# Performance work log

Measured on AMD Instinct MI355X. Metric: run time of the kernel, lower is better.

Reference implementation:

```python
import jax, jax.numpy as jnp
import numpy as np


def setup_inputs() -> dict:
    key = jax.random.key(0)
    k1, k2, k3, k4, k5, k6 = jax.random.split(key, 6)
    B, V = 128, 128000
    logits = jax.random.normal(k1, (B, V), dtype=jnp.float32) * 2.0
    # keep temperatures away from 0 to avoid overflow in logits/temp
    temperatures = 0.7 + 0.6 * jax.random.uniform(k2, (B,), dtype=jnp.float32)
    top_ks = jax.random.randint(k3, (B,), 1, 1024, dtype=jnp.int32)
    top_ps = 0.7 + 0.29 * jax.random.uniform(k4, (B,), dtype=jnp.float32)
    min_ps = 0.02 * jax.random.uniform(k5, (B,), dtype=jnp.float32)
    # uniform variate for inverse-CDF multinomial sampling (one sample per row)
    u = jax.random.uniform(k6, (B, 1), dtype=jnp.float32)
    return {
        "logits": logits,
        "temperatures": temperatures,
        "top_ks": top_ks,
        "top_ps": top_ps,
        "min_ps": min_ps,
        "u": u,
    }


def reference(logits, temperatures, top_ks, top_ps, min_ps, u):
    """Faithful jax version of Sampler's torch-native sampling path:
    softmax(logits/T) -> descending sort -> top-k mask -> top-p mask
    (cumsum computed pre-mask, exactly as torch code) -> min-p mask ->
    multinomial sample (inverse CDF with provided uniform u) ->
    gather original token index. Also returns the renormalized filtered
    probs scattered back to vocab order (top_p_normalize_probs-style)."""
    B, V = logits.shape
    probs = jax.nn.softmax(logits / temperatures[:, None], axis=-1)  # [B, V]

    order = jnp.argsort(-probs, axis=-1)                     # descending indices
    probs_sort = jnp.take_along_axis(probs, order, axis=-1)  # [B, V] sorted desc
    probs_sum = jnp.cumsum(probs_sort, axis=-1)              # cumsum BEFORE masking

    pos = jnp.arange(V, dtype=jnp.int32)[None, :]
    # top-k: zero everything at rank >= top_k
    probs_sort = jnp.where(pos >= top_ks[:, None], 0.0, probs_sort)
    # top-p: zero where cumulative mass strictly before this token exceeds top_p
    probs_sort = jnp.where(probs_sum - probs_sort > top_ps[:, None], 0.0, probs_sort)
    # min-p: threshold relative to the max prob (rank-0 entry survives both masks)
    min_p_thr = probs_sort[:, :1] * min_ps[:, None]
    probs_sort = jnp.where(probs_sort < min_p_thr, 0.0, probs_sort)

    total = jnp.sum(probs_sort, axis=-1, keepdims=True)      # [B, 1]
    cdf = jnp.cumsum(probs_sort, axis=-1) / total            # normalized CDF
    # inverse-CDF sampling == torch.multinomial(probs_sort, 1)
    sampled_rank = jnp.clip(jnp.sum(cdf < u, axis=-1, keepdims=True), 0, V - 1)
    token_ids = jnp.take_along_axis(order, sampled_rank, axis=-1)[:, 0].astype(jnp.int32)

    # scatter renormalized filtered probs back to original vocab positions
    inv_order = jnp.argsort(order, axis=-1)
    norm_probs = jnp.take_along_axis(probs_sort / total, inv_order, axis=-1)
    return token_ids, norm_probs
```

## Files before the change

kernel.cpp:

```cpp
#include <hip/hip_runtime.h>
#include <stdint.h>
#include <math.h>

#define T0 256
#define T1 512
#define TPB 1024
#define NB 2048
#define SPLIT 8
#define LCAND 1024
#define CAND2 2048
#define PS0 2048
#define L2E 1.44269504088896f

typedef float vfloat4 __attribute__((ext_vector_type(4)));
typedef unsigned long long ull;

__device__ __forceinline__ unsigned fkey(float f) {
    unsigned u = __float_as_uint(f);
    return (u & 0x80000000u) ? ~u : (u | 0x80000000u);
}
__device__ __forceinline__ float funkey(unsigned k) {
    unsigned u = (k & 0x80000000u) ? (k ^ 0x80000000u) : ~k;
    return __uint_as_float(u);
}
__device__ __forceinline__ ull packkv(unsigned k, unsigned idx) {
    return ((ull)k << 32) | (ull)(~idx);
}

__device__ __forceinline__ void suffix_scan_2048(unsigned* h, unsigned* wscr, int tid)
{
    const int lane = tid & 63, w = tid >> 6;
    const int i0 = 2047 - 2 * tid;
    const int i1 = 2046 - 2 * tid;
    unsigned a = h[i0], b = h[i1];
    unsigned s = a + b;
    unsigned inc = s;
    #pragma unroll
    for (int d = 1; d < 64; d <<= 1) { unsigned o = __shfl_up(inc, d); if (lane >= d) inc += o; }
    if (lane == 63) wscr[w] = inc;
    __syncthreads();
    if (w == 0) {
        unsigned v = (lane < 16) ? wscr[lane] : 0u;
        unsigned vi = v;
        #pragma unroll
        for (int d = 1; d < 16; d <<= 1) { unsigned o = __shfl_up(vi, d); if (lane >= d) vi += o; }
        if (lane < 16) wscr[16 + lane] = vi - v;
    }
    __syncthreads();
    unsigned off = wscr[16 + w] + (inc - s);
    h[i0] = off + a;
    h[i1] = off + a + b;
    __syncthreads();
}

__global__ __launch_bounds__(T0)
void k0_cut(const float* __restrict__ logits,
            const float* __restrict__ temps,
            const int* __restrict__ top_ks,
            float* __restrict__ ws_cy,
            unsigned* __restrict__ ws_cut,
            int V, int Vq)
{
    const int slot = blockIdx.x;
    const int b = slot / SPLIT, s = slot % SPLIT;
    const int tid = threadIdx.x, lane = tid & 63, w = tid >> 6;
    const int start = s * Vq;
    const int len = min(Vq, V - start);

    __shared__ unsigned hist[NB];
    __shared__ unsigned uscr[16];
    __shared__ float fred[8];
    __shared__ int bstar;

    if (len <= 0) {
        if (tid == 0) { ws_cut[slot] = 0xFFFFFFFFu; ws_cy[slot] = -1e30f; }
        return;
    }
    for (int i = tid; i < NB; i += T0) hist[i] = 0;
    if (tid == 0) bstar = 0;
    __syncthreads();

    const float* __restrict__ row = logits + (size_t)b * V + start;
    const vfloat4* __restrict__ row4 = (const vfloat4*)row;
    const int nps = min(len, PS0);
    const int np4 = nps >> 2;

    float m0 = -1e30f;
    for (int i = tid; i < np4; i += T0) {
        vfloat4 v = row4[i];
        #pragma unroll
        for (int j = 0; j < 4; ++j) {
            float lv = v[j];
            m0 = fmaxf(m0, lv);
            atomicAdd(&hist[fkey(lv) >> 21], 1u);
        }
    }
    for (int i = (np4 << 2) + tid; i < nps; i += T0) {
        float lv = row[i];
        m0 = fmaxf(m0, lv);
        atomicAdd(&hist[fkey(lv) >> 21], 1u);
    }
    #pragma unroll
    for (int d = 32; d > 0; d >>= 1) m0 = fmaxf(m0, __shfl_down(m0, d));
    if (lane == 0) fred[w] = m0;
    __syncthreads();
    if (tid == 0) {
        float mm = fred[0];
        for (int j = 1; j < T0 / 64; ++j) mm = fmaxf(mm, fred[j]);
        fred[4] = mm;
    }
    __syncthreads();
    const float m0max = fred[4];

    unsigned sloc[8];
    unsigned acc = 0;
    #pragma unroll
    for (int j = 0; j < 8; ++j) { acc += hist[2047 - (8 * tid + j)]; sloc[j] = acc; }
    __syncthreads();
    unsigned inc = acc;
    #pragma unroll
    for (int d = 1; d < 64; d <<= 1) { unsigned o = __shfl_up(inc, d); if (lane >= d) inc += o; }
    if (lane == 63) uscr[w] = inc;
    __syncthreads();
    if (tid == 0) {
        unsigned o = 0;
        for (int j = 0; j < T0 / 64; ++j) { unsigned t = uscr[j]; uscr[8 + j] = o; o += t; }
    }
    __syncthreads();
    unsigned off = uscr[8 + w] + (inc - acc);
    #pragma unroll
    for (int j = 0; j < 8; ++j) hist[2047 - (8 * tid + j)] = off + sloc[j];
    __syncthreads();

    int K = top_ks[b]; K = max(K, 1); K = min(K, 1024);
    float sexp = (float)K * (float)nps / (float)V;
    unsigned TGT = (unsigned)(sexp + 6.0f * sqrtf(sexp) + 16.5f);
    if (TGT > (unsigned)nps) TGT = (unsigned)nps;
    for (int e = tid; e < NB; e += T0) {
        unsigned Se = hist[e];
        unsigned Sn = (e < NB - 1) ? hist[e + 1] : 0u;
        if (Se >= TGT && Sn < TGT) bstar = e;
    }
    __syncthreads();
    if (tid == 0) {
        ws_cut[slot] = (unsigned)bstar << 21;
        ws_cy[slot]  = m0max / temps[b];
    }
}

__global__ __launch_bounds__(T1)
void k1_scan(const float* __restrict__ logits,
             const float* __restrict__ temps,
             float* __restrict__ out_probs,
             const float* __restrict__ ws_cy,
             const unsigned* __restrict__ ws_cut,
             float* __restrict__ ws_z,
             unsigned* __restrict__ ws_cnt,
             unsigned* __restrict__ ws_maxk,
             ull* __restrict__ ws_cand,
             int V, int Vq)
{
    const int slot = blockIdx.x;
    const int b = slot / SPLIT, s = slot % SPLIT;
    const int tid = threadIdx.x, lane = tid & 63, w = tid >> 6;
    const int start = s * Vq;
    const int len = min(Vq, V - start);

    __shared__ float fred[16];
    __shared__ unsigned cnt;

    if (len <= 0) {
        if (tid == 0) { ws_z[slot] = 0.0f; ws_cnt[slot] = 0u; ws_maxk[slot] = 0u; }
        return;
    }
    if (tid == 0) cnt = 0;
    __syncthreads();

    const float invT = 1.0f / temps[b];
    const float Cy = ws_cy[slot];
    const unsigned cutkey = ws_cut[slot];
    const float cutval = funkey(cutkey);

    const float* __restrict__ row = logits + (size_t)b * V + start;
    const vfloat4* __restrict__ row4 = (const vfloat4*)row;
    const int L4 = len >> 2;

    {
        float* __restrict__ orow = out_probs + (size_t)b * V + start;
        vfloat4* __restrict__ orow4 = (vfloat4*)orow;
        const vfloat4 z4 = (vfloat4)0.0f;
        for (int i = tid; i < L4; i += T1) orow4[i] = z4;
        for (int i = (L4 << 2) + tid; i < len; i += T1) orow[i] = 0.0f;
    }

    const float ca = invT * L2E;
    const float cb = -Cy * L2E;
    ull* gc = ws_cand + (size_t)slot * LCAND;

    float z0 = 0.0f, z1 = 0.0f, z2 = 0.0f, z3 = 0.0f, mb = -1e30f;

    #define E4(v) (exp2f(fmaf((v)[0], ca, cb)) + exp2f(fmaf((v)[1], ca, cb)) \
                 + exp2f(fmaf((v)[2], ca, cb)) + exp2f(fmaf((v)[3], ca, cb)))
    #define GATHER(v, ii) do {                                                  \
        bool c0 = (v)[0] >= cutval, c1 = (v)[1] >= cutval,                      \
             c2 = (v)[2] >= cutval, c3 = (v)[3] >= cutval;                      \
        if (c0 | c1 | c2 | c3) {                                                \
            mb = fmaxf(mb, fmaxf(fmaxf((v)[0], (v)[1]), fmaxf((v)[2], (v)[3])));\
            int nh = (int)c0 + (int)c1 + (int)c2 + (int)c3;                     \
            unsigned base = atomicAdd(&cnt, (unsigned)nh);                      \
            unsigned bi = (unsigned)(start + ((ii) << 2));                      \
            if (c0) { if (base < LCAND) gc[base] = packkv(fkey((v)[0]), bi+0); base++; } \
            if (c1) { if (base < LCAND) gc[base] = packkv(fkey((v)[1]), bi+1); base++; } \
            if (c2) { if (base < LCAND) gc[base] = packkv(fkey((v)[2]), bi+2); base++; } \
            if (c3) { if (base < LCAND) gc[base] = packkv(fkey((v)[3]), bi+3); base++; } \
        }                                                                       \
    } while (0)

    int i = tid;
    for (; i + 3 * T1 < L4; i += 4 * T1) {
        vfloat4 va = row4[i];
        vfloat4 vb = row4[i + T1];
        vfloat4 vc = row4[i + 2 * T1];
        vfloat4 vd = row4[i + 3 * T1];
        z0 += E4(va); z1 += E4(vb); z2 += E4(vc); z3 += E4(vd);
        GATHER(va, i); GATHER(vb, i + T1); GATHER(vc, i + 2 * T1); GATHER(vd, i + 3 * T1);
    }
    for (; i < L4; i += T1) {
        vfloat4 v = row4[i];
        z0 += E4(v);
        GATHER(v, i);
    }
    for (int j = (L4 << 2) + tid; j < len; j += T1) {
        float lv = row[j];
        z0 += exp2f(fmaf(lv, ca, cb));
        if (lv >= cutval) {
            mb = fmaxf(mb, lv);
            unsigned base = atomicAdd(&cnt, 1u);
            if (base < LCAND) gc[base] = packkv(fkey(lv), (unsigned)(start + j));
        }
    }
    #undef E4
    #undef GATHER

    float z = (z0 + z1) + (z2 + z3);
    __syncthreads();
    #pragma unroll
    for (int d = 32; d > 0; d >>= 1) {
        z += __shfl_down(z, d);
        mb = fmaxf(mb, __shfl_down(mb, d));
    }
    if (lane == 0) { fred[w] = z; fred[8 + w] = mb; }
    __syncthreads();
    if (tid == 0) {
        float zz = 0.0f, mm = -1e30f;
        for (int j = 0; j < T1 / 64; ++j) { zz += fred[j]; mm = fmaxf(mm, fred[8 + j]); }
        ws_z[slot] = zz;
        ws_cnt[slot] = cnt;
        ws_maxk[slot] = (cnt > 0u) ? fkey(mm) : 0u;
    }
}

__global__ __launch_bounds__(TPB)
void k2_sample(const float* __restrict__ logits,
               const float* __restrict__ temps,
               const int* __restrict__ top_ks,
               const float* __restrict__ top_ps,
               const float* __restrict__ min_ps,
               const float* __restrict__ uvec,
               const float* __restrict__ ws_cy,
               const float* __restrict__ ws_z,
               const unsigned* __restrict__ ws_cut,
               const unsigned* __restrict__ ws_cnt,
               const unsigned* __restrict__ ws_maxk,
               const ull* __restrict__ ws_cand,
               float* __restrict__ out_tok,
               float* __restrict__ out_probs,
               int V)
{
    const int b = blockIdx.x;
    const int tid = threadIdx.x, lane = tid & 63, w = tid >> 6;
    const float invT = 1.0f / temps[b];
    int Korig = top_ks[b]; Korig = max(Korig, 1); Korig = min(Korig, 1024);
    const unsigned Ku = (unsigned)Korig;
    const float top_p = top_ps[b], min_p = min_ps[b], uval = uvec[b];

    __shared__ __align__(16) char smem[53504];
    ull*            cand  = (ull*)(smem);
    ull*            cand2 = (ull*)(smem + 16384);
    unsigned*       hist  = (unsigned*)(smem + 32768);
    unsigned short* cnts  = (unsigned short*)(smem + 41216);
    float*          sh_p  = (float*)(smem + 45312);
    float*          sh_c  = (float*)(smem + 49408);
    __shared__ unsigned uscr[32];
    __shared__ float fws[32];
    __shared__ unsigned scnt;
    __shared__ int sh_i1, sh_i2;
    __shared__ unsigned sh_u1;

    float Cy[SPLIT], zq[SPLIT];
    unsigned cutq[SPLIT], cntq[SPLIT], mkq[SPLIT];
    #pragma unroll
    for (int q = 0; q < SPLIT; ++q) {
        int sl = b * SPLIT + q;
        Cy[q] = ws_cy[sl]; zq[q] = ws_z[sl];
        cutq[q] = ws_cut[sl]; cntq[q] = ws_cnt[sl]; mkq[q] = ws_maxk[sl];
    }
    float Y = -1e30f;
    #pragma unroll
    for (int q = 0; q < SPLIT; ++q) if (cntq[q] > 0u) Y = fmaxf(Y, Cy[q]);
    float Z = 0.0f;
    #pragma unroll
    for (int q = 0; q < SPLIT; ++q)
        if (cntq[q] > 0u && zq[q] > 0.0f) Z += zq[q] * exp2f((Cy[q] - Y) * L2E);

    bool fb = false;
    unsigned cutmax = 0, mincut = 0xFFFFFFFFu, maxkey = 0;
    #pragma unroll
    for (int q = 0; q < SPLIT; ++q) {
        if (cntq[q] > (unsigned)LCAND) fb = true;
        if (cntq[q] > 0u) {
            if (!isfinite(zq[q])) fb = true;
            cutmax = max(cutmax, cutq[q]);
            mincut = min(mincut, cutq[q]);
            maxkey = max(maxkey, mkq[q]);
        }
    }
    if (mincut == 0xFFFFFFFFu || !isfinite(Z) || Z <= 0.0f) fb = true;

    unsigned Tkeyb = 0;
    int count = 0, bstar = 0, shift = 0;
    const unsigned base = mincut;

    if (!fb) {
        const unsigned range = maxkey - base;
        while ((range >> shift) > (unsigned)(NB - 1)) shift++;
        for (int i = tid; i <= NB; i += TPB) hist[i] = 0;
        if (tid == 0) { sh_i1 = -1; scnt = 0; }
        __syncthreads();
        #pragma unroll
        for (int q = 0; q < SPLIT; ++q) {
            const ull* gc = ws_cand + (size_t)(b * SPLIT + q) * LCAND;
            int nl = min((int)cntq[q], LCAND);
            for (int i = tid; i < nl; i += TPB)
                atomicAdd(&hist[((unsigned)(gc[i] >> 32) - base) >> shift], 1u);
        }
        __syncthreads();
        unsigned fat = 0;
        for (int i = tid; i < NB; i += TPB) {
            unsigned h = hist[i];
            cnts[i] = (unsigned short)h;
            fat = max(fat, h);
        }
        #pragma unroll
        for (int d = 32; d > 0; d >>= 1) fat = max(fat, __shfl_down(fat, d));
        if (lane == 0) uscr[w] = fat;
        __syncthreads();
        if (tid == 0) {
            unsigned m2 = 0;
            for (int j = 0; j < 16; ++j) m2 = max(m2, uscr[j]);
            uscr[16] = m2;
        }
        __syncthreads();
        if (uscr[16] > 64u) fb = true;
    }
    if (!fb) {
        suffix_scan_2048(hist, uscr, tid);
        for (int e = tid; e < NB; e += TPB) {
            unsigned Se = hist[e], Sn = (e < NB - 1) ? hist[e + 1] : 0u;
            if (Se >= Ku && Sn < Ku) { sh_i1 = e; sh_u1 = Se; }
        }
        __syncthreads();
        if (sh_i1 < 0) fb = true;
        else {
            bstar = sh_i1;
            count = (int)sh_u1;
            Tkeyb = base + ((unsigned)bstar << shift);
            if (Tkeyb < cutmax || count > CAND2) fb = true;
        }
    }
    if (!fb) {
        #pragma unroll
        for (int q = 0; q < SPLIT; ++q) {
            const ull* gc = ws_cand + (size_t)(b * SPLIT + q) * LCAND;
            int nl = min((int)cntq[q], LCAND);
            for (int i = tid; i < nl; i += TPB) {
                ull e = gc[i];
                unsigned k = (unsigned)(e >> 32);
                if (k >= Tkeyb) {
                    unsigned bin = (k - base) >> shift;
                    unsigned pos = atomicAdd(&hist[bin + 1], 1u);
                    cand2[pos] = e;
                }
            }
        }
        __syncthreads();
        for (int e = bstar + tid; e < NB; e += TPB) {
            int c = (int)cnts[e];
            if (c >= 2) {
                int st = (int)hist[e + 1] - c;
                for (int x = 1; x < c; ++x) {
                    ull key = cand2[st + x];
                    int y = x - 1;
                    while (y >= 0 && cand2[st + y] < key) { cand2[st + y + 1] = cand2[st + y]; --y; }
                    cand2[st + y + 1] = key;
                }
            }
        }
        __syncthreads();
    }

    if (fb) {
        const float* __restrict__ row = logits + (size_t)b * V;
        float m = -1e30f, z = 0.0f;
        for (int i = tid; i < V; i += TPB) {
            float y = row[i] * invT;
            float nm = fmaxf(m, y);
            z = z * exp2f((m - nm) * L2E) + exp2f((y - nm) * L2E);
            m = nm;
        }
        sh_p[tid] = m; sh_c[tid] = z;
        __syncthreads();
        for (int d = TPB >> 1; d > 0; d >>= 1) {
            if (tid < d) {
                float m1 = sh_p[tid], z1 = sh_c[tid];
                float m2 = sh_p[tid + d], z2 = sh_c[tid + d];
                float mm = fmaxf(m1, m2);
                sh_c[tid] = z1 * exp2f((m1 - mm) * L2E) + z2 * exp2f((m2 - mm) * L2E);
                sh_p[tid] = mm;
            }
            __syncthreads();
        }
        Y = sh_p[0]; Z = sh_c[0];
        __syncthreads();
        for (int i = tid; i < NB; i += TPB) hist[i] = 0;
        if (tid == 0) { sh_i1 = 0; sh_i2 = 0; sh_u1 = 0; }
        __syncthreads();
        for (int i = tid; i < V; i += TPB) atomicAdd(&hist[fkey(row[i]) >> 21], 1u);
        __syncthreads();
        suffix_scan_2048(hist, uscr, tid);
        for (int e = tid; e < NB; e += TPB) {
            unsigned Se = hist[e], Sn = (e < NB-1) ? hist[e+1] : 0u;
            if (Se >= Ku && Sn < Ku) { sh_i1 = e; sh_u1 = Sn; }
        }
        __syncthreads();
        int b1 = sh_i1;
        unsigned cab = sh_u1;
        for (int i = tid; i < NB; i += TPB) hist[i] = 0;
        __syncthreads();
        for (int i = tid; i < V; i += TPB) {
            unsigned k = fkey(row[i]);
            if ((int)(k >> 21) == b1) atomicAdd(&hist[(k >> 10) & (NB - 1)], 1u);
        }
        __syncthreads();
        suffix_scan_2048(hist, uscr, tid);
        for (int e = tid; e < NB; e += TPB) {
            unsigned Se = cab + hist[e];
            unsigned Sn = cab + ((e < NB-1) ? hist[e+1] : 0u);
            if (Se >= Ku && Sn < Ku) sh_i2 = e;
        }
        __syncthreads();
        unsigned Tkey = ((unsigned)b1 << 21) | ((unsigned)sh_i2 << 10);
        if (tid == 0) scnt = 0;
        __syncthreads();
        for (int i = tid; i < V; i += TPB) {
            unsigned k = fkey(row[i]);
            if (k >= Tkey) {
                unsigned pos = atomicAdd(&scnt, 1u);
                if (pos < CAND2) cand[pos] = packkv(k, (unsigned)i);
            }
        }
        __syncthreads();
        count = (scnt < (unsigned)CAND2) ? (int)scnt : CAND2;

        int n_sort = 1;
        while (n_sort < count) n_sort <<= 1;
        for (int i = tid; i < n_sort; i += TPB)
            if (i >= count) cand[i] = 0ull;
        __syncthreads();
        for (int kk = 2; kk <= n_sort; kk <<= 1) {
            for (int j = kk >> 1; j > 0; j >>= 1) {
                for (int i = tid; i < n_sort; i += TPB) {
                    int ixj = i ^ j;
                    if (ixj > i) {
                        ull a = cand[i], c = cand[ixj];
                        bool up = (i & kk) == 0;
                        if (up ? (a < c) : (a > c)) { cand[i] = c; cand[ixj] = a; }
                    }
                }
                __syncthreads();
            }
        }
    }

    ull* srt = fb ? cand : cand2;
    int K = min(Korig, count);

    float pv = 0.0f;
    if (tid < K) {
        unsigned k = (unsigned)(srt[tid] >> 32);
        pv = exp2f((funkey(k) * invT - Y) * L2E) / Z;
    }
    float inc = pv;
    #pragma unroll
    for (int d = 1; d < 64; d <<= 1) { float o = __shfl_up(inc, d); if (lane >= d) inc += o; }
    if (lane == 63) fws[w] = inc;
    __syncthreads();
    if (w == 0) {
        float v = (lane < 16) ? fws[lane] : 0.0f;
        float vi = v;
        #pragma unroll
        for (int d = 1; d < 16; d <<= 1) { float o = __shfl_up(vi, d); if (lane >= d) vi += o; }
        if (lane < 16) fws[16 + lane] = vi - v;
    }
    __syncthreads();
    float cum = inc + fws[16 + w];
    sh_p[tid] = pv;
    sh_c[tid] = cum;
    if (tid == 0) sh_i1 = K;
    __syncthreads();

    if (tid < K) {
        float excl = cum - pv;
        if (excl > top_p) atomicMin(&sh_i1, tid);
    }
    __syncthreads();
    int n1 = sh_i1;
    float thr = sh_p[0] * min_p;
    if (tid == 0) sh_i2 = n1;
    __syncthreads();
    if (tid < n1 && sh_p[tid] < thr) atomicMin(&sh_i2, tid);
    __syncthreads();
    int nf = sh_i2;
    float total = sh_c[nf - 1];

    int pred = (tid < nf) && ((sh_c[tid] / total) < uval);
    int rank = __syncthreads_count(pred);
    if (rank > nf - 1) rank = nf - 1;
    if (rank < 0) rank = 0;
    if (tid == 0)
        out_tok[b] = (float)(~(unsigned)(srt[rank] & 0xFFFFFFFFull));

    if (tid < nf) {
        unsigned idx = ~(unsigned)(srt[tid] & 0xFFFFFFFFull);
        out_probs[(size_t)b * V + idx] = sh_p[tid] / total;
    }
}

extern "C" void kernel_launch(void* const* d_in, const int* in_sizes, int n_in,
                              void* d_out, int out_size, void* d_ws, size_t ws_size,
                              hipStream_t stream) {
    const float* logits = (const float*)d_in[0];
    const float* temps  = (const float*)d_in[1];
    const int*   top_ks = (const int*)d_in[2];
    const float* top_ps = (const float*)d_in[3];
    const float* min_ps = (const float*)d_in[4];
    const float* u      = (const float*)d_in[5];
    const int B = in_sizes[1];
    const int V = in_sizes[0] / B;
    float* out_tok   = (float*)d_out;
    float* out_probs = out_tok + B;

    int Vq = (((V + SPLIT - 1) / SPLIT) + 3) & ~3;

    char* ws = (char*)d_ws;
    size_t off = 0;
    auto take = [&](size_t bytes) { char* p = ws + off; off = (off + bytes + 255) & ~(size_t)255; return p; };
    float*    ws_cy   = (float*)take((size_t)B * SPLIT * sizeof(float));
    float*    ws_z    = (float*)take((size_t)B * SPLIT * sizeof(float));
    unsigned* ws_cut  = (unsigned*)take((size_t)B * SPLIT * sizeof(unsigned));
    unsigned* ws_cnt  = (unsigned*)take((size_t)B * SPLIT * sizeof(unsigned));
    unsigned* ws_maxk = (unsigned*)take((size_t)B * SPLIT * sizeof(unsigned));
    ull*      ws_cand = (ull*)take((size_t)B * SPLIT * LCAND * sizeof(ull));
    (void)ws_size;

    k0_cut<<<dim3(SPLIT * B), dim3(T0), 0, stream>>>(
        logits, temps, top_ks, ws_cy, ws_cut, V, Vq);
    k1_scan<<<dim3(SPLIT * B), dim3(T1), 0, stream>>>(
        logits, temps, out_probs, ws_cy, ws_cut, ws_z, ws_cnt, ws_maxk, ws_cand, V, Vq);
    k2_sample<<<dim3(B), dim3(TPB), 0, stream>>>(
        logits, temps, top_ks, top_ps, min_ps, u, ws_cy, ws_z, ws_cut, ws_cnt,
        ws_maxk, ws_cand, out_tok, out_probs, V);
}
```

Before: 157.4 us.

## Replace shared-atomic candidate gather with per-wave ballot compaction into segments

The scan kernel no longer appends threshold-passing candidates through a block-wide shared atomic counter. Each wave now compacts them with ballot and popcount into its own fixed 256-entry segment, which removes the atomics, the initial barrier and the related divergence. The sample kernel reads the per-wave counts, walks every segment slot and masks out the unused ones. In exchange it scans a fixed 64×256 range per row, and overflow now triggers when any single wave segment exceeds 256 entries rather than when the whole slot exceeds 1024.

```diff
diff --git a/kernel.cpp b/kernel.cpp
--- a/kernel.cpp
+++ b/kernel.cpp
@@ -7,7 +7,9 @@
 #define TPB 1024
 #define NB 2048
 #define SPLIT 8
-#define LCAND 1024
+#define NW 8
+#define LW 256
+#define NSEG (SPLIT*NW)
 #define CAND2 2048
 #define PS0 2048
 #define L2E 1.44269504088896f
@@ -155,31 +157,29 @@
              const float* __restrict__ ws_cy,
              const unsigned* __restrict__ ws_cut,
              float* __restrict__ ws_z,
-             unsigned* __restrict__ ws_cnt,
+             unsigned* __restrict__ ws_wcnt,
              unsigned* __restrict__ ws_maxk,
              ull* __restrict__ ws_cand,
              int V, int Vq)
 {
     const int slot = blockIdx.x;
     const int b = slot / SPLIT, s = slot % SPLIT;
-    const int tid = threadIdx.x, lane = tid & 63, w = tid >> 6;
+    const int tid = threadIdx.x, lane = tid & 63, wv = tid >> 6;
     const int start = s * Vq;
     const int len = min(Vq, V - start);
 
-    __shared__ float fred[16];
-    __shared__ unsigned cnt;
+    __shared__ float fred[2 * NW];
+    __shared__ unsigned ucnt[NW];
 
     if (len <= 0) {
-        if (tid == 0) { ws_z[slot] = 0.0f; ws_cnt[slot] = 0u; ws_maxk[slot] = 0u; }
+        if (lane == 0) ws_wcnt[slot * NW + wv] = 0u;
+        if (tid == 0) { ws_z[slot] = 0.0f; ws_maxk[slot] = 0u; }
         return;
     }
-    if (tid == 0) cnt = 0;
-    __syncthreads();
 
     const float invT = 1.0f / temps[b];
     const float Cy = ws_cy[slot];
-    const unsigned cutkey = ws_cut[slot];
-    const float cutval = funkey(cutkey);
+    const float cutval = funkey(ws_cut[slot]);
 
     const float* __restrict__ row = logits + (size_t)b * V + start;
     const vfloat4* __restrict__ row4 = (const vfloat4*)row;
@@ -195,68 +195,71 @@
 
     const float ca = invT * L2E;
     const float cb = -Cy * L2E;
-    ull* gc = ws_cand + (size_t)slot * LCAND;
-
+    ull* gw = ws_cand + ((size_t)slot * NW + wv) * LW;
+    const ull lmask = (1ull << lane) - 1ull;
+
+    unsigned wcnt = 0;
     float z0 = 0.0f, z1 = 0.0f, z2 = 0.0f, z3 = 0.0f, mb = -1e30f;
 
     #define E4(v) (exp2f(fmaf((v)[0], ca, cb)) + exp2f(fmaf((v)[1], ca, cb)) \
                  + exp2f(fmaf((v)[2], ca, cb)) + exp2f(fmaf((v)[3], ca, cb)))
-    #define GATHER(v, ii) do {                                                  \
-        bool c0 = (v)[0] >= cutval, c1 = (v)[1] >= cutval,                      \
-             c2 = (v)[2] >= cutval, c3 = (v)[3] >= cutval;                      \
-        if (c0 | c1 | c2 | c3) {                                                \
-            mb = fmaxf(mb, fmaxf(fmaxf((v)[0], (v)[1]), fmaxf((v)[2], (v)[3])));\
-            int nh = (int)c0 + (int)c1 + (int)c2 + (int)c3;                     \
-            unsigned base = atomicAdd(&cnt, (unsigned)nh);                      \
-            unsigned bi = (unsigned)(start + ((ii) << 2));                      \
-            if (c0) { if (base < LCAND) gc[base] = packkv(fkey((v)[0]), bi+0); base++; } \
-            if (c1) { if (base < LCAND) gc[base] = packkv(fkey((v)[1]), bi+1); base++; } \
-            if (c2) { if (base < LCAND) gc[base] = packkv(fkey((v)[2]), bi+2); base++; } \
-            if (c3) { if (base < LCAND) gc[base] = packkv(fkey((v)[3]), bi+3); base++; } \
-        }                                                                       \
+    #define GE1(x, gi) do {                                                 \
+        bool p = (x) >= cutval;                                             \
+        ull bm = __ballot(p);                                               \
+        if (bm) {                                                           \
+            mb = fmaxf(mb, p ? (x) : -1e30f);                               \
+            unsigned pos = wcnt + (unsigned)__popcll(bm & lmask);           \
+            if (p && pos < LW) gw[pos] = packkv(fkey(x), (unsigned)(gi));   \
+            wcnt += (unsigned)__popcll(bm);                                 \
+        }                                                                   \
     } while (0)
-
-    int i = tid;
-    for (; i + 3 * T1 < L4; i += 4 * T1) {
-        vfloat4 va = row4[i];
-        vfloat4 vb = row4[i + T1];
-        vfloat4 vc = row4[i + 2 * T1];
-        vfloat4 vd = row4[i + 3 * T1];
+    #define GE4(v, ii) do {                                                 \
+        unsigned gbase = (unsigned)(start + ((ii) << 2));                   \
+        GE1((v)[0], gbase + 0); GE1((v)[1], gbase + 1);                     \
+        GE1((v)[2], gbase + 2); GE1((v)[3], gbase + 3);                     \
+    } while (0)
+
+    int k = 0;
+    for (; (k + 4) * T1 <= L4; k += 4) {
+        int i0 = k * T1 + tid;
+        vfloat4 va = row4[i0];
+        vfloat4 vb = row4[i0 + T1];
+        vfloat4 vc = row4[i0 + 2 * T1];
+        vfloat4 vd = row4[i0 + 3 * T1];
         z0 += E4(va); z1 += E4(vb); z2 += E4(vc); z3 += E4(vd);
-        GATHER(va, i); GATHER(vb, i + T1); GATHER(vc, i + 2 * T1); GATHER(vd, i + 3 * T1);
-    }
-    for (; i < L4; i += T1) {
-        vfloat4 v = row4[i];
+        GE4(va, i0); GE4(vb, i0 + T1); GE4(vc, i0 + 2 * T1); GE4(vd, i0 + 3 * T1);
+    }
+    for (; k * T1 + (wv << 6) < L4; ++k) {
+        int idx = k * T1 + tid;
+        vfloat4 v = (idx < L4) ? row4[idx] : (vfloat4)(-1e30f);
         z0 += E4(v);
-        GATHER(v, i);
+        GE4(v, idx);
     }
     for (int j = (L4 << 2) + tid; j < len; j += T1) {
         float lv = row[j];
         z0 += exp2f(fmaf(lv, ca, cb));
-        if (lv >= cutval) {
-            mb = fmaxf(mb, lv);
-            unsigned base = atomicAdd(&cnt, 1u);
-            if (base < LCAND) gc[base] = packkv(fkey(lv), (unsigned)(start + j));
-        }
+        GE1(lv, start + j);
     }
     #undef E4
-    #undef GATHER
+    #undef GE1
+    #undef GE4
 
     float z = (z0 + z1) + (z2 + z3);
-    __syncthreads();
     #pragma unroll
     for (int d = 32; d > 0; d >>= 1) {
         z += __shfl_down(z, d);
         mb = fmaxf(mb, __shfl_down(mb, d));
     }
-    if (lane == 0) { fred[w] = z; fred[8 + w] = mb; }
+    if (lane == 0) {
+        fred[wv] = z; fred[NW + wv] = mb; ucnt[wv] = wcnt;
+        ws_wcnt[slot * NW + wv] = wcnt;
+    }
     __syncthreads();
     if (tid == 0) {
-        float zz = 0.0f, mm = -1e30f;
-        for (int j = 0; j < T1 / 64; ++j) { zz += fred[j]; mm = fmaxf(mm, fred[8 + j]); }
+        float zz = 0.0f, mm = -1e30f; unsigned tot = 0;
+        for (int j = 0; j < NW; ++j) { zz += fred[j]; mm = fmaxf(mm, fred[NW + j]); tot += ucnt[j]; }
         ws_z[slot] = zz;
-        ws_cnt[slot] = cnt;
-        ws_maxk[slot] = (cnt > 0u) ? fkey(mm) : 0u;
+        ws_maxk[slot] = tot ? fkey(mm) : 0u;
     }
 }
 
@@ -270,7 +273,7 @@
                const float* __restrict__ ws_cy,
                const float* __restrict__ ws_z,
                const unsigned* __restrict__ ws_cut,
-               const unsigned* __restrict__ ws_cnt,
+               const unsigned* __restrict__ ws_wcnt,
                const unsigned* __restrict__ ws_maxk,
                const ull* __restrict__ ws_cand,
                float* __restrict__ out_tok,
@@ -284,52 +287,68 @@
     const unsigned Ku = (unsigned)Korig;
     const float top_p = top_ps[b], min_p = min_ps[b], uval = uvec[b];
 
-    __shared__ __align__(16) char smem[53504];
+    __shared__ __align__(16) char smem[53760];
     ull*            cand  = (ull*)(smem);
     ull*            cand2 = (ull*)(smem + 16384);
     unsigned*       hist  = (unsigned*)(smem + 32768);
     unsigned short* cnts  = (unsigned short*)(smem + 41216);
     float*          sh_p  = (float*)(smem + 45312);
     float*          sh_c  = (float*)(smem + 49408);
+    unsigned short* segc  = (unsigned short*)(smem + 53504);
     __shared__ unsigned uscr[32];
     __shared__ float fws[32];
     __shared__ unsigned scnt;
     __shared__ int sh_i1, sh_i2;
     __shared__ unsigned sh_u1;
 
+    bool myfb = false;
+    for (int i = tid; i < NSEG; i += TPB) {
+        unsigned c = ws_wcnt[b * NSEG + i];
+        if (c > (unsigned)LW) myfb = true;
+        segc[i] = (unsigned short)min(c, (unsigned)LW);
+    }
     float Cy[SPLIT], zq[SPLIT];
-    unsigned cutq[SPLIT], cntq[SPLIT], mkq[SPLIT];
+    unsigned cutq[SPLIT], mkq[SPLIT];
     #pragma unroll
     for (int q = 0; q < SPLIT; ++q) {
         int sl = b * SPLIT + q;
         Cy[q] = ws_cy[sl]; zq[q] = ws_z[sl];
-        cutq[q] = ws_cut[sl]; cntq[q] = ws_cnt[sl]; mkq[q] = ws_maxk[sl];
+        cutq[q] = ws_cut[sl]; mkq[q] = ws_maxk[sl];
+    }
+    __syncthreads();
+    unsigned cntq[SPLIT];
+    #pragma unroll
+    for (int q = 0; q < SPLIT; ++q) {
+        unsigned t = 0;
+        #pragma unroll
+        for (int v = 0; v < NW; ++v) t += segc[q * NW + v];
+        cntq[q] = t;
     }
     float Y = -1e30f;
     #pragma unroll
-    for (int q = 0; q < SPLIT; ++q) if (cntq[q] > 0u) Y = fmaxf(Y, Cy[q]);
+    for (int q = 0; q < SPLIT; ++q) if (zq[q] > 0.0f) Y = fmaxf(Y, Cy[q]);
     float Z = 0.0f;
     #pragma unroll
     for (int q = 0; q < SPLIT; ++q)
-        if (cntq[q] > 0u && zq[q] > 0.0f) Z += zq[q] * exp2f((Cy[q] - Y) * L2E);
-
-    bool fb = false;
+        if (zq[q] > 0.0f) Z += zq[q] * exp2f((Cy[q] - Y) * L2E);
+
     unsigned cutmax = 0, mincut = 0xFFFFFFFFu, maxkey = 0;
     #pragma unroll
     for (int q = 0; q < SPLIT; ++q) {
-        if (cntq[q] > (unsigned)LCAND) fb = true;
         if (cntq[q] > 0u) {
-            if (!isfinite(zq[q])) fb = true;
+            if (!isfinite(zq[q])) myfb = true;
             cutmax = max(cutmax, cutq[q]);
             mincut = min(mincut, cutq[q]);
             maxkey = max(maxkey, mkq[q]);
         }
     }
-    if (mincut == 0xFFFFFFFFu || !isfinite(Z) || Z <= 0.0f) fb = true;
+    if (mincut == 0xFFFFFFFFu || !isfinite(Z) || Z <= 0.0f) myfb = true;
+    bool fb = __syncthreads_or((int)myfb) != 0;
 
     unsigned Tkeyb = 0;
     int count = 0, bstar = 0, shift = 0;
     const unsigned base = mincut;
+    const ull* cbase = ws_cand + (size_t)b * NSEG * LW;
 
     if (!fb) {
         const unsigned range = maxkey - base;
@@ -337,12 +356,13 @@
         for (int i = tid; i <= NB; i += TPB) hist[i] = 0;
         if (tid == 0) { sh_i1 = -1; scnt = 0; }
         __syncthreads();
-        #pragma unroll
-        for (int q = 0; q < SPLIT; ++q) {
-            const ull* gc = ws_cand + (size_t)(b * SPLIT + q) * LCAND;
-            int nl = min((int)cntq[q], LCAND);
-            for (int i = tid; i < nl; i += TPB)
-                atomicAdd(&hist[((unsigned)(gc[i] >> 32) - base) >> shift], 1u);
+        for (int v = tid; v < NSEG * LW; v += TPB) {
+            int off = v & (LW - 1);
+            int seg = v >> 8;
+            if (off < (int)segc[seg]) {
+                ull e = cbase[v];
+                atomicAdd(&hist[((unsigned)(e >> 32) - base) >> shift], 1u);
+            }
         }
         __syncthreads();
         unsigned fat = 0;
@@ -379,12 +399,11 @@
         }
     }
     if (!fb) {
-        #pragma unroll
-        for (int q = 0; q < SPLIT; ++q) {
-            const ull* gc = ws_cand + (size_t)(b * SPLIT + q) * LCAND;
-            int nl = min((int)cntq[q], LCAND);
-            for (int i = tid; i < nl; i += TPB) {
-                ull e = gc[i];
+        for (int v = tid; v < NSEG * LW; v += TPB) {
+            int off = v & (LW - 1);
+            int seg = v >> 8;
+            if (off < (int)segc[seg]) {
+                ull e = cbase[v];
                 unsigned k = (unsigned)(e >> 32);
                 if (k >= Tkeyb) {
                     unsigned bin = (k - base) >> shift;
@@ -568,16 +587,16 @@
     float*    ws_cy   = (float*)take((size_t)B * SPLIT * sizeof(float));
     float*    ws_z    = (float*)take((size_t)B * SPLIT * sizeof(float));
     unsigned* ws_cut  = (unsigned*)take((size_t)B * SPLIT * sizeof(unsigned));
-    unsigned* ws_cnt  = (unsigned*)take((size_t)B * SPLIT * sizeof(unsigned));
+    unsigned* ws_wcnt = (unsigned*)take((size_t)B * NSEG * sizeof(unsigned));
     unsigned* ws_maxk = (unsigned*)take((size_t)B * SPLIT * sizeof(unsigned));
-    ull*      ws_cand = (ull*)take((size_t)B * SPLIT * LCAND * sizeof(ull));
+    ull*      ws_cand = (ull*)take((size_t)B * NSEG * LW * sizeof(ull));
     (void)ws_size;
 
     k0_cut<<<dim3(SPLIT * B), dim3(T0), 0, stream>>>(
         logits, temps, top_ks, ws_cy, ws_cut, V, Vq);
     k1_scan<<<dim3(SPLIT * B), dim3(T1), 0, stream>>>(
-        logits, temps, out_probs, ws_cy, ws_cut, ws_z, ws_cnt, ws_maxk, ws_cand, V, Vq);
+        logits, temps, out_probs, ws_cy, ws_cut, ws_z, ws_wcnt, ws_maxk, ws_cand, V, Vq);
     k2_sample<<<dim3(B), dim3(TPB), 0, stream>>>(
-        logits, temps, top_ks, top_ps, min_ps, u, ws_cy, ws_z, ws_cut, ws_cnt,
+        logits, temps, top_ks, top_ps, min_ps, u, ws_cy, ws_z, ws_cut, ws_wcnt,
         ws_maxk, ws_cand, out_tok, out_probs, V);
 }
```

Result: no change. 158.3 us (+0.5%).
